# Kernel optimization log

Hardware: AMD Instinct MI355X
Metric: run time of the kernel (lower is better)

Reference implementation:

```python
import jax, jax.numpy as jnp
import numpy as np

B, LQ, C = 2, 12240, 256
NH, NL, NP = 8, 4, 4          # heads, levels, points
D = C // NH                   # head dim = 32
SHAPES = np.array([[96, 96], [48, 48], [24, 24], [12, 12]], dtype=np.int32)
LEN_IN = int((SHAPES[:, 0] * SHAPES[:, 1]).sum())  # 12240


def setup_inputs() -> dict:
    key = jax.random.key(0)
    ks = jax.random.split(key, 10)
    start = np.concatenate([[0], np.cumsum(SHAPES[:, 0] * SHAPES[:, 1])[:-1]]).astype(np.int32)
    return {
        "query": jax.random.normal(ks[0], (B, LQ, C), jnp.float32),
        "reference_points": jax.random.uniform(ks[1], (B, LQ, NL, 2), jnp.float32),
        "input_flatten": jax.random.normal(ks[2], (B, LEN_IN, C), jnp.float32),
        "input_spatial_shapes": jnp.asarray(SHAPES),
        "input_level_start_index": jnp.asarray(start),
        # params (sampling_offsets weight kept small so samples land near the reference point)
        "W_off": jax.random.normal(ks[3], (C, NH * NL * NP * 2), jnp.float32) * 0.01,
        "b_off": jax.random.normal(ks[4], (NH * NL * NP * 2,), jnp.float32) * 0.1,
        "W_attn": jax.random.normal(ks[5], (C, NH * NL * NP), jnp.float32) * 0.02,
        "b_attn": jnp.zeros((NH * NL * NP,), jnp.float32),
        "W_val": jax.random.normal(ks[6], (C, C), jnp.float32) * (1.0 / np.sqrt(C)),
        "b_val": jnp.zeros((C,), jnp.float32),
        "W_out": jax.random.normal(ks[7], (C, C), jnp.float32) * (1.0 / np.sqrt(C)),
        "b_out": jnp.zeros((C,), jnp.float32),
    }


def _bilinear_sample(v, loc):
    """grid_sample(align_corners=False, padding=zeros) equivalent.
    v:   (B, Hl, Wl, NH, D) level feature map per head
    loc: (B, Lq, NH, NP, 2) normalized sampling locations in [0,1]
    ->   (B, Lq, NH, NP, D)
    """
    _, Hl, Wl, _, _ = v.shape
    x = loc[..., 0] * Wl - 0.5
    y = loc[..., 1] * Hl - 0.5
    x0 = jnp.floor(x); y0 = jnp.floor(y)
    lx = x - x0;       ly = y - y0
    x0i = x0.astype(jnp.int32); y0i = y0.astype(jnp.int32)
    bi = jnp.arange(v.shape[0])[:, None, None, None]
    hi = jnp.arange(NH)[None, None, :, None]

    def gather(yi, xi):
        valid = (yi >= 0) & (yi < Hl) & (xi >= 0) & (xi < Wl)
        yc = jnp.clip(yi, 0, Hl - 1)
        xc = jnp.clip(xi, 0, Wl - 1)
        g = v[bi, yc, xc, hi]                       # (B,Lq,NH,NP,D)
        return g * valid[..., None].astype(v.dtype)

    w00 = (1 - lx) * (1 - ly); w01 = lx * (1 - ly)
    w10 = (1 - lx) * ly;       w11 = lx * ly
    return (gather(y0i, x0i) * w00[..., None] + gather(y0i, x0i + 1) * w01[..., None]
            + gather(y0i + 1, x0i) * w10[..., None] + gather(y0i + 1, x0i + 1) * w11[..., None])


def reference(query, reference_points, input_flatten, input_spatial_shapes,
              input_level_start_index, W_off, b_off, W_attn, b_attn,
              W_val, b_val, W_out, b_out):
    shapes = np.asarray(input_spatial_shapes)          # static level geometry
    starts = np.asarray(input_level_start_index)

    value = (input_flatten @ W_val + b_val).reshape(B, LEN_IN, NH, D)
    offsets = (query @ W_off + b_off).reshape(B, LQ, NH, NL, NP, 2)
    attn = (query @ W_attn + b_attn).reshape(B, LQ, NH, NL * NP)
    attn = jax.nn.softmax(attn, axis=-1).reshape(B, LQ, NH, NL, NP)

    # normalizer is (W_l, H_l) per level
    normalizer = jnp.stack([input_spatial_shapes[:, 1], input_spatial_shapes[:, 0]], -1).astype(query.dtype)
    loc = (reference_points[:, :, None, :, None, :]
           + offsets / normalizer[None, None, None, :, None, :])  # (B,Lq,NH,NL,NP,2)

    out = jnp.zeros((B, LQ, NH, D), query.dtype)
    for l in range(NL):
        Hl, Wl = int(shapes[l, 0]), int(shapes[l, 1])
        s = int(starts[l])
        v_l = value[:, s:s + Hl * Wl].reshape(B, Hl, Wl, NH, D)
        sampled = _bilinear_sample(v_l, loc[:, :, :, l])            # (B,Lq,NH,NP,D)
        out = out + jnp.einsum("bqhpd,bqhp->bqhd", sampled, attn[:, :, :, l])
    out = out.reshape(B, LQ, C)
    return out @ W_out + b_out
```

## Files before the change

kernel.cpp:

```cpp
#include <hip/hip_runtime.h>
#include <math.h>

#define B_    2
#define LQ_   12240
#define C_    256
#define NH_   8
#define NL_   4
#define NP_   4
#define LEN_IN_ 12240
#define MROWS (B_*LQ_)
#define MF_   (MROWS/16)
#define KF_   8
#define APLANE ((size_t)MROWS * C_)
#define NBLK  383

typedef __attribute__((ext_vector_type(8))) short short8v;
typedef __attribute__((ext_vector_type(4))) float f32x4;
typedef __attribute__((ext_vector_type(2))) float f32x2;
typedef __attribute__((ext_vector_type(2))) uint  u32x2;

__device__ __forceinline__ ushort f2bf_hi(float f) {
    uint u = __builtin_bit_cast(uint, f);
    uint r = (u + 0x7fffu + ((u >> 16) & 1u)) >> 16;
    return (ushort)r;
}
__device__ __forceinline__ float bf2f(ushort h) {
    uint u = ((uint)h) << 16;
    return __builtin_bit_cast(float, u);
}

#define U4_VAL  0
#define U4_OFF  8192
#define U4_ATT  16384
#define U4_UHI  20480
#define U4_ULO  28672
#define PACKB_TOTAL 294912

#define ESTRIDE 272
#define FSTRIDE 268

__global__ __launch_bounds__(256) void pack_w_kernel(
    const float* __restrict__ Wv, const float* __restrict__ Wo,
    const float* __restrict__ Wa, const float* __restrict__ Wu,
    ushort* __restrict__ packB)
{
    int gid = blockIdx.x * 256 + threadIdx.x;
    if (gid >= 28672) return;
    const float* W; ushort* hi; ushort* lo = nullptr; int N, rel;
    if (gid < 8192)       { W = Wv; hi = packB;          N = 256; rel = gid; }
    else if (gid < 16384) { W = Wo; hi = packB + 65536;  N = 256; rel = gid - 8192; }
    else if (gid < 20480) { W = Wa; hi = packB + 131072; N = 128; rel = gid - 16384; }
    else { W = Wu; hi = packB + 163840; lo = packB + 229376; N = 256; rel = gid - 20480; }

    const int lane = rel & 63;
    const int kf   = (rel >> 6) & 7;
    const int nf   = rel >> 9;
    const int row0 = kf * 32 + (lane >> 4) * 8;
    const int col  = nf * 16 + (lane & 15);

    union { ushort u16[8]; uint4 u4; } ch, cl;
#pragma unroll
    for (int j = 0; j < 8; ++j) {
        float x = W[(size_t)(row0 + j) * N + col];
        ushort h = f2bf_hi(x);
        ch.u16[j] = h;
        cl.u16[j] = f2bf_hi(x - bf2f(h));
    }
    *reinterpret_cast<uint4*>(hi + (size_t)rel * 8) = ch.u4;
    if (lo) *reinterpret_cast<uint4*>(lo + (size_t)rel * 8) = cl.u4;
}

__global__ __launch_bounds__(512) void gemm_vq_kernel(
    const float* __restrict__ inflat, const float* __restrict__ query,
    const ushort* __restrict__ packB,
    const float* __restrict__ b_val, const float* __restrict__ b_off,
    const float* __restrict__ b_attn,
    ushort* __restrict__ valbf, ushort* __restrict__ offsb, ushort* __restrict__ attnb)
{
    const int t = threadIdx.x, lane = t & 63, wid = t >> 6;
    const int rowBase = blockIdx.x * 64;
    const bool isVal = (blockIdx.y == 0);
    const float* __restrict__ A = isVal ? inflat : query;

    __shared__ ushort Sh[64 * ESTRIDE];

#pragma unroll
    for (int i = 0; i < 4; ++i) {
        int frag = i * 512 + t;
        int fl = frag & 63, kf = (frag >> 6) & 7, mf = frag >> 9;
        int row = min(rowBase + mf * 16 + (fl & 15), MROWS - 1);
        int k0 = kf * 32 + (fl >> 4) * 8;
        const float4* s = reinterpret_cast<const float4*>(A + (size_t)row * 256 + k0);
        float4 v0 = s[0], v1 = s[1];
        float vv[8] = { v0.x, v0.y, v0.z, v0.w, v1.x, v1.y, v1.z, v1.w };
        union { ushort u16[8]; uint4 u4; } hh;
#pragma unroll
        for (int j = 0; j < 8; ++j) hh.u16[j] = f2bf_hi(vv[j]);
        *reinterpret_cast<uint4*>(&Sh[(size_t)frag * 8]) = hh.u4;
    }
    __syncthreads();

    const uint4* A4 = reinterpret_cast<const uint4*>(Sh);
    const int colLane = lane & 15, rquad = lane >> 4;
    const int wnf = wid * 2;

    if (isVal) {
        const uint4* B4 = reinterpret_cast<const uint4*>(packB) + U4_VAL;
        f32x4 acc[4][2];
#pragma unroll
        for (int mi = 0; mi < 4; ++mi)
#pragma unroll
            for (int f = 0; f < 2; ++f) acc[mi][f] = (f32x4)0.0f;

#pragma unroll
        for (int kf = 0; kf < KF_; ++kf) {
            uint4 bh[2], ah[4];
#pragma unroll
            for (int f = 0; f < 2; ++f) bh[f] = B4[((wnf + f) * KF_ + kf) * 64 + lane];
#pragma unroll
            for (int mi = 0; mi < 4; ++mi) ah[mi] = A4[(mi * KF_ + kf) * 64 + lane];
#pragma unroll
            for (int mi = 0; mi < 4; ++mi) {
                short8v a = __builtin_bit_cast(short8v, ah[mi]);
#pragma unroll
                for (int f = 0; f < 2; ++f)
                    acc[mi][f] = __builtin_amdgcn_mfma_f32_16x16x32_bf16(
                        a, __builtin_bit_cast(short8v, bh[f]), acc[mi][f], 0, 0, 0);
            }
        }
        __syncthreads();
#pragma unroll
        for (int f = 0; f < 2; ++f) {
            int col = (wnf + f) * 16 + colLane;
            float bv = b_val[col];
#pragma unroll
            for (int mi = 0; mi < 4; ++mi)
#pragma unroll
                for (int e = 0; e < 4; ++e)
                    Sh[(mi * 16 + rquad * 4 + e) * ESTRIDE + col] = f2bf_hi(acc[mi][f][e] + bv);
        }
        __syncthreads();
#pragma unroll
        for (int i = 0; i < 4; ++i) {
            int idx = i * 512 + t, row = idx >> 5, c8 = idx & 31;
            int grow = rowBase + row;
            if (grow < MROWS)
                *reinterpret_cast<uint4*>(valbf + (size_t)grow * 256 + c8 * 8) =
                    *reinterpret_cast<const uint4*>(&Sh[row * ESTRIDE + c8 * 8]);
        }
    } else {
        const uint4* BO = reinterpret_cast<const uint4*>(packB) + U4_OFF;
        const uint4* BA = reinterpret_cast<const uint4*>(packB) + U4_ATT;
        f32x4 acc[4][3];
#pragma unroll
        for (int mi = 0; mi < 4; ++mi)
#pragma unroll
            for (int f = 0; f < 3; ++f) acc[mi][f] = (f32x4)0.0f;

#pragma unroll
        for (int kf = 0; kf < KF_; ++kf) {
            uint4 bh[3], ah[4];
#pragma unroll
            for (int f = 0; f < 2; ++f) bh[f] = BO[((wnf + f) * KF_ + kf) * 64 + lane];
            bh[2] = BA[(wid * KF_ + kf) * 64 + lane];
#pragma unroll
            for (int mi = 0; mi < 4; ++mi) ah[mi] = A4[(mi * KF_ + kf) * 64 + lane];
#pragma unroll
            for (int mi = 0; mi < 4; ++mi) {
                short8v a = __builtin_bit_cast(short8v, ah[mi]);
#pragma unroll
                for (int f = 0; f < 3; ++f)
                    acc[mi][f] = __builtin_amdgcn_mfma_f32_16x16x32_bf16(
                        a, __builtin_bit_cast(short8v, bh[f]), acc[mi][f], 0, 0, 0);
            }
        }
        __syncthreads();
#pragma unroll
        for (int f = 0; f < 2; ++f) {
            int col = (wnf + f) * 16 + colLane;
            float bv = b_off[col];
#pragma unroll
            for (int mi = 0; mi < 4; ++mi)
#pragma unroll
                for (int e = 0; e < 4; ++e)
                    Sh[(mi * 16 + rquad * 4 + e) * ESTRIDE + col] = f2bf_hi(acc[mi][f][e] + bv);
        }
        __syncthreads();
#pragma unroll
        for (int i = 0; i < 4; ++i) {
            int idx = i * 512 + t, row = idx >> 5, c8 = idx & 31;
            int grow = rowBase + row;
            if (grow < MROWS)
                *reinterpret_cast<uint4*>(offsb + (size_t)grow * 256 + c8 * 8) =
                    *reinterpret_cast<const uint4*>(&Sh[row * ESTRIDE + c8 * 8]);
        }
        __syncthreads();
        {
            int col = wid * 16 + colLane;
            float bv = b_attn[col];
#pragma unroll
            for (int mi = 0; mi < 4; ++mi)
#pragma unroll
                for (int e = 0; e < 4; ++e) {
                    float v = acc[mi][2][e] + bv;
                    float mx = v;
#pragma unroll
                    for (int m = 8; m >= 1; m >>= 1) mx = fmaxf(mx, __shfl_xor(mx, m, 16));
                    float ex = __expf(v - mx);
                    float s = ex;
#pragma unroll
                    for (int m = 8; m >= 1; m >>= 1) s += __shfl_xor(s, m, 16);
                    Sh[(mi * 16 + rquad * 4 + e) * ESTRIDE + col] = f2bf_hi(ex / s);
                }
        }
        __syncthreads();
#pragma unroll
        for (int i = 0; i < 2; ++i) {
            int idx = i * 512 + t, row = idx >> 4, c8 = idx & 15;
            int grow = rowBase + row;
            if (grow < MROWS)
                *reinterpret_cast<uint4*>(attnb + (size_t)grow * 128 + c8 * 8) =
                    *reinterpret_cast<const uint4*>(&Sh[row * ESTRIDE + c8 * 8]);
        }
    }
}

__global__ __launch_bounds__(512) void gemm_out_kernel(
    const ushort* __restrict__ midH, const ushort* __restrict__ packB,
    const float* __restrict__ bias, float* __restrict__ Cg)
{
    const int t = threadIdx.x, lane = t & 63, wid = t >> 6;
    const int rowBase = blockIdx.x * 64;

    __shared__ ushort Sh[64 * ESTRIDE];

    const uint4* H4 = reinterpret_cast<const uint4*>(midH);
#pragma unroll
    for (int i = 0; i < 4; ++i) {
        int frag = i * 512 + t;
        int fl = frag & 63, kf = (frag >> 6) & 7, mf = frag >> 9;
        int row = min(rowBase + mf * 16 + (fl & 15), MROWS - 1);
        int kq = kf * 4 + (fl >> 4);
        *reinterpret_cast<uint4*>(&Sh[(size_t)frag * 8]) = H4[(size_t)row * 32 + kq];
    }
    __syncthreads();

    const uint4* BH4 = reinterpret_cast<const uint4*>(packB) + U4_UHI;
    const uint4* BL4 = reinterpret_cast<const uint4*>(packB) + U4_ULO;
    const uint4* A4 = reinterpret_cast<const uint4*>(Sh);
    const int wnf = wid * 2;

    f32x4 acc[4][2];
#pragma unroll
    for (int mi = 0; mi < 4; ++mi)
#pragma unroll
        for (int f = 0; f < 2; ++f) acc[mi][f] = (f32x4)0.0f;

#pragma unroll
    for (int kf = 0; kf < KF_; ++kf) {
        uint4 bh[2], bl[2], ah[4];
#pragma unroll
        for (int f = 0; f < 2; ++f) {
            bh[f] = BH4[((wnf + f) * KF_ + kf) * 64 + lane];
            bl[f] = BL4[((wnf + f) * KF_ + kf) * 64 + lane];
        }
#pragma unroll
        for (int mi = 0; mi < 4; ++mi) ah[mi] = A4[(mi * KF_ + kf) * 64 + lane];
#pragma unroll
        for (int mi = 0; mi < 4; ++mi) {
            short8v a = __builtin_bit_cast(short8v, ah[mi]);
#pragma unroll
            for (int f = 0; f < 2; ++f) {
                acc[mi][f] = __builtin_amdgcn_mfma_f32_16x16x32_bf16(
                    a, __builtin_bit_cast(short8v, bh[f]), acc[mi][f], 0, 0, 0);
                acc[mi][f] = __builtin_amdgcn_mfma_f32_16x16x32_bf16(
                    a, __builtin_bit_cast(short8v, bl[f]), acc[mi][f], 0, 0, 0);
            }
        }
    }

    const int colLane = lane & 15, rquad = lane >> 4;
    float* ShF = reinterpret_cast<float*>(Sh);
#pragma unroll
    for (int phase = 0; phase < 2; ++phase) {
        __syncthreads();
#pragma unroll
        for (int f = 0; f < 2; ++f) {
            int col = (wnf + f) * 16 + colLane;
            float bv = bias[col];
#pragma unroll
            for (int mi2 = 0; mi2 < 2; ++mi2) {
                int mi = phase * 2 + mi2;
#pragma unroll
                for (int e = 0; e < 4; ++e)
                    ShF[(mi2 * 16 + rquad * 4 + e) * FSTRIDE + col] = acc[mi][f][e] + bv;
            }
        }
        __syncthreads();
#pragma unroll
        for (int i = 0; i < 4; ++i) {
            int idx = i * 512 + t, row = idx >> 6, c4 = idx & 63;
            int grow = rowBase + phase * 32 + row;
            if (grow < MROWS)
                *reinterpret_cast<float4*>(Cg + (size_t)grow * 256 + c4 * 4) =
                    *reinterpret_cast<const float4*>(&ShF[row * FSTRIDE + c4 * 4]);
        }
    }
}

__global__ __launch_bounds__(128) void sampler_kernel(
    const ushort* __restrict__ value,
    const ushort* __restrict__ offs,
    const ushort* __restrict__ attnw,
    const float* __restrict__ refp,
    ushort* __restrict__ midH)
{
    const int t  = threadIdx.x;
    const int qi = t >> 6;
    const int t6 = t & 63;
    const int q  = blockIdx.x * 2 + qi;

    __shared__ float s_ref[2][8];
    __shared__ int   s_addr[2][576];
    __shared__ float s_w[2][576];

    if (t < 16) s_ref[t >> 3][t & 7] = refp[(size_t)(blockIdx.x * 2 + (t >> 3)) * 8 + (t & 7)];
    __syncthreads();

#pragma unroll
    for (int batch = 0; batch < 2; ++batch) {
        const int p  = t6 + batch * 64;
        const int h  = p >> 4;
        const int lp = p & 15;
        const int l  = lp >> 2;

        const float aw = bf2f(attnw[(size_t)q * 128 + p]);
        const uint o2 = reinterpret_cast<const uint*>(offs)[(size_t)q * 128 + p];
        const float ox = bf2f((ushort)(o2 & 0xffffu));
        const float oy = bf2f((ushort)(o2 >> 16));
        const float rx = s_ref[qi][l * 2 + 0];
        const float ry = s_ref[qi][l * 2 + 1];

        const int   Wl = 96 >> l;
        const int   st = 12288 - (12288 >> (2 * l));
        const float fW = (float)Wl;

        const float x = fmaf(rx, fW, ox) - 0.5f;
        const float y = fmaf(ry, fW, oy) - 0.5f;
        const float x0f = floorf(x), y0f = floorf(y);
        const float fx = x - x0f, fy = y - y0f;
        const int x0 = (int)x0f, y0 = (int)y0f;
        const int x1 = x0 + 1,   y1 = y0 + 1;

        const float vx0 = (x0 >= 0 && x0 < Wl) ? 1.f : 0.f;
        const float vx1 = (x1 >= 0 && x1 < Wl) ? 1.f : 0.f;
        const float vy0 = (y0 >= 0 && y0 < Wl) ? 1.f : 0.f;
        const float vy1 = (y1 >= 0 && y1 < Wl) ? 1.f : 0.f;

        const int xc0 = min(max(x0, 0), Wl - 1);
        const int xc1 = min(max(x1, 0), Wl - 1);
        const int yc0 = min(max(y0, 0), Wl - 1);
        const int yc1 = min(max(y1, 0), Wl - 1);

        const int row0 = st + yc0 * Wl;
        const int row1 = st + yc1 * Wl;
        const int hb   = h << 5;

        const int sidx = (lp * 9 + h) * 4;
        int4 a;
        a.x = ((row0 + xc0) << 8) + hb;
        a.y = ((row0 + xc1) << 8) + hb;
        a.z = ((row1 + xc0) << 8) + hb;
        a.w = ((row1 + xc1) << 8) + hb;
        *reinterpret_cast<int4*>(&s_addr[qi][sidx]) = a;

        float4 w;
        w.x = aw * (1.f - fx) * (1.f - fy) * vx0 * vy0;
        w.y = aw * fx * (1.f - fy) * vx1 * vy0;
        w.z = aw * (1.f - fx) * fy * vx0 * vy1;
        w.w = aw * fx * fy * vx1 * vy1;
        *reinterpret_cast<float4*>(&s_w[qi][sidx]) = w;
    }
    __syncthreads();

    const int c2 = t6 >> 5;
    const int h  = (t6 >> 2) & 7;
    const int l2 = t6 & 3;
    const int d8 = l2 * 8;
    const ushort* __restrict__ vb = value + (q >= LQ_ ? (size_t)LEN_IN_ * 256 : 0) + d8;

    f32x2 aLo = (f32x2)0.f, aHi = (f32x2)0.f, bLo = (f32x2)0.f, bHi = (f32x2)0.f;

#pragma unroll
    for (int pt = 0; pt < 16; ++pt) {
        const int base = (pt * 9 + h) * 4 + c2 * 2;
        const int2   a = *reinterpret_cast<const int2*>(&s_addr[qi][base]);
        const float2 w = *reinterpret_cast<const float2*>(&s_w[qi][base]);
        uint4 v0 = *reinterpret_cast<const uint4*>(vb + a.x);
        uint4 v1 = *reinterpret_cast<const uint4*>(vb + a.y);
        f32x2 w0; w0.x = w.x; w0.y = w.x;
        f32x2 w1; w1.x = w.y; w1.y = w.y;

        u32x2 h01; h01.x = v0.x; h01.y = v0.y;
        u32x2 h23; h23.x = v0.z; h23.y = v0.w;
        u32x2 l01 = h01 << 16, l23 = h23 << 16;
        aHi = __builtin_elementwise_fma(__builtin_bit_cast(f32x2, h01), w0, aHi);
        aLo = __builtin_elementwise_fma(__builtin_bit_cast(f32x2, l01), w0, aLo);
        bHi = __builtin_elementwise_fma(__builtin_bit_cast(f32x2, h23), w0, bHi);
        bLo = __builtin_elementwise_fma(__builtin_bit_cast(f32x2, l23), w0, bLo);

        u32x2 g01; g01.x = v1.x; g01.y = v1.y;
        u32x2 g23; g23.x = v1.z; g23.y = v1.w;
        u32x2 m01 = g01 << 16, m23 = g23 << 16;
        aHi = __builtin_elementwise_fma(__builtin_bit_cast(f32x2, g01), w1, aHi);
        aLo = __builtin_elementwise_fma(__builtin_bit_cast(f32x2, m01), w1, aLo);
        bHi = __builtin_elementwise_fma(__builtin_bit_cast(f32x2, g23), w1, bHi);
        bLo = __builtin_elementwise_fma(__builtin_bit_cast(f32x2, m23), w1, bLo);
    }

    float r[8] = { aLo.x, aHi.x, aLo.y, aHi.y, bLo.x, bHi.x, bLo.y, bHi.y };
#pragma unroll
    for (int j = 0; j < 8; ++j) r[j] += __shfl_xor(r[j], 32);

    if (c2 == 0) {
        union { ushort u16[8]; uint4 u4; } hh;
#pragma unroll
        for (int j = 0; j < 8; ++j) hh.u16[j] = f2bf_hi(r[j]);
        *reinterpret_cast<uint4*>(midH + (size_t)q * 256 + (h << 5) + d8) = hh.u4;
    }
}

extern "C" void kernel_launch(void* const* d_in, const int* in_sizes, int n_in,
                              void* d_out, int out_size, void* d_ws, size_t ws_size,
                              hipStream_t stream)
{
    const float* query  = (const float*)d_in[0];
    const float* refp   = (const float*)d_in[1];
    const float* inflat = (const float*)d_in[2];
    const float* W_off  = (const float*)d_in[5];
    const float* b_off  = (const float*)d_in[6];
    const float* W_attn = (const float*)d_in[7];
    const float* b_attn = (const float*)d_in[8];
    const float* W_val  = (const float*)d_in[9];
    const float* b_val  = (const float*)d_in[10];
    const float* W_out  = (const float*)d_in[11];
    const float* b_out  = (const float*)d_in[12];
    float* out = (float*)d_out;

    ushort* midH  = (ushort*)d_ws;
    ushort* valbf = midH + APLANE;
    ushort* packB = valbf + APLANE;
    ushort* offsb = packB + PACKB_TOTAL;
    ushort* attnb = offsb + APLANE;

    hipLaunchKernelGGL(pack_w_kernel, dim3(112), dim3(256), 0, stream,
                       W_val, W_off, W_attn, W_out, packB);
    hipLaunchKernelGGL(gemm_vq_kernel, dim3(NBLK, 2), dim3(512), 0, stream,
                       inflat, query, packB, b_val, b_off, b_attn,
                       valbf, offsb, attnb);
    hipLaunchKernelGGL(sampler_kernel, dim3(MROWS / 2), dim3(128), 0, stream,
                       valbf, offsb, attnb, refp, midH);
    hipLaunchKernelGGL(gemm_out_kernel, dim3(NBLK), dim3(512), 0, stream,
                       midH, packB, b_out, out);
}
```

Measured before the change: 79.87 us.

## Fuse deformable sampler with output projection GEMM in one kernel

Merges the sampling kernel and the output-projection GEMM into one kernel that handles 16 queries per block. The sampled bf16 head outputs stay in shared memory and feed MFMA directly, which removes the global round trip through the intermediate buffer and one kernel launch. Sampling weights are now stored in shared memory as bf16 to save LDS, at some cost in precision. The GEMM tile shrinks to 16 rows per block, so each block reloads the full weight matrix, and the larger LDS footprint may reduce occupancy.

Result: slower. 83.44 us (+4.5%).

```diff
diff --git a/kernel.cpp b/kernel.cpp
--- a/kernel.cpp
+++ b/kernel.cpp
@@ -9,10 +9,10 @@
 #define NP_   4
 #define LEN_IN_ 12240
 #define MROWS (B_*LQ_)
-#define MF_   (MROWS/16)
 #define KF_   8
 #define APLANE ((size_t)MROWS * C_)
 #define NBLK  383
+#define QBLK  1530
 
 typedef __attribute__((ext_vector_type(8))) short short8v;
 typedef __attribute__((ext_vector_type(4))) float f32x4;
@@ -37,7 +37,8 @@
 #define PACKB_TOTAL 294912
 
 #define ESTRIDE 272
-#define FSTRIDE 268
+#define MSTRIDE 264
+#define OSTRIDE 260
 
 __global__ __launch_bounds__(256) void pack_w_kernel(
     const float* __restrict__ Wv, const float* __restrict__ Wo,
@@ -225,121 +226,42 @@
     }
 }
 
-__global__ __launch_bounds__(512) void gemm_out_kernel(
-    const ushort* __restrict__ midH, const ushort* __restrict__ packB,
-    const float* __restrict__ bias, float* __restrict__ Cg)
-{
-    const int t = threadIdx.x, lane = t & 63, wid = t >> 6;
-    const int rowBase = blockIdx.x * 64;
-
-    __shared__ ushort Sh[64 * ESTRIDE];
-
-    const uint4* H4 = reinterpret_cast<const uint4*>(midH);
-#pragma unroll
-    for (int i = 0; i < 4; ++i) {
-        int frag = i * 512 + t;
-        int fl = frag & 63, kf = (frag >> 6) & 7, mf = frag >> 9;
-        int row = min(rowBase + mf * 16 + (fl & 15), MROWS - 1);
-        int kq = kf * 4 + (fl >> 4);
-        *reinterpret_cast<uint4*>(&Sh[(size_t)frag * 8]) = H4[(size_t)row * 32 + kq];
-    }
-    __syncthreads();
-
-    const uint4* BH4 = reinterpret_cast<const uint4*>(packB) + U4_UHI;
-    const uint4* BL4 = reinterpret_cast<const uint4*>(packB) + U4_ULO;
-    const uint4* A4 = reinterpret_cast<const uint4*>(Sh);
-    const int wnf = wid * 2;
-
-    f32x4 acc[4][2];
-#pragma unroll
-    for (int mi = 0; mi < 4; ++mi)
-#pragma unroll
-        for (int f = 0; f < 2; ++f) acc[mi][f] = (f32x4)0.0f;
-
-#pragma unroll
-    for (int kf = 0; kf < KF_; ++kf) {
-        uint4 bh[2], bl[2], ah[4];
-#pragma unroll
-        for (int f = 0; f < 2; ++f) {
-            bh[f] = BH4[((wnf + f) * KF_ + kf) * 64 + lane];
-            bl[f] = BL4[((wnf + f) * KF_ + kf) * 64 + lane];
-        }
-#pragma unroll
-        for (int mi = 0; mi < 4; ++mi) ah[mi] = A4[(mi * KF_ + kf) * 64 + lane];
-#pragma unroll
-        for (int mi = 0; mi < 4; ++mi) {
-            short8v a = __builtin_bit_cast(short8v, ah[mi]);
-#pragma unroll
-            for (int f = 0; f < 2; ++f) {
-                acc[mi][f] = __builtin_amdgcn_mfma_f32_16x16x32_bf16(
-                    a, __builtin_bit_cast(short8v, bh[f]), acc[mi][f], 0, 0, 0);
-                acc[mi][f] = __builtin_amdgcn_mfma_f32_16x16x32_bf16(
-                    a, __builtin_bit_cast(short8v, bl[f]), acc[mi][f], 0, 0, 0);
-            }
-        }
-    }
-
-    const int colLane = lane & 15, rquad = lane >> 4;
-    float* ShF = reinterpret_cast<float*>(Sh);
-#pragma unroll
-    for (int phase = 0; phase < 2; ++phase) {
-        __syncthreads();
-#pragma unroll
-        for (int f = 0; f < 2; ++f) {
-            int col = (wnf + f) * 16 + colLane;
-            float bv = bias[col];
-#pragma unroll
-            for (int mi2 = 0; mi2 < 2; ++mi2) {
-                int mi = phase * 2 + mi2;
-#pragma unroll
-                for (int e = 0; e < 4; ++e)
-                    ShF[(mi2 * 16 + rquad * 4 + e) * FSTRIDE + col] = acc[mi][f][e] + bv;
-            }
-        }
-        __syncthreads();
-#pragma unroll
-        for (int i = 0; i < 4; ++i) {
-            int idx = i * 512 + t, row = idx >> 6, c4 = idx & 63;
-            int grow = rowBase + phase * 32 + row;
-            if (grow < MROWS)
-                *reinterpret_cast<float4*>(Cg + (size_t)grow * 256 + c4 * 4) =
-                    *reinterpret_cast<const float4*>(&ShF[row * FSTRIDE + c4 * 4]);
-        }
-    }
-}
-
-__global__ __launch_bounds__(128) void sampler_kernel(
+__global__ __launch_bounds__(512) void sampler_out_kernel(
     const ushort* __restrict__ value,
     const ushort* __restrict__ offs,
     const ushort* __restrict__ attnw,
     const float* __restrict__ refp,
-    ushort* __restrict__ midH)
+    const ushort* __restrict__ packB,
+    const float* __restrict__ b_out,
+    float* __restrict__ outp)
 {
-    const int t  = threadIdx.x;
-    const int qi = t >> 6;
-    const int t6 = t & 63;
-    const int q  = blockIdx.x * 2 + qi;
-
-    __shared__ float s_ref[2][8];
-    __shared__ int   s_addr[2][576];
-    __shared__ float s_w[2][576];
-
-    if (t < 16) s_ref[t >> 3][t & 7] = refp[(size_t)(blockIdx.x * 2 + (t >> 3)) * 8 + (t & 7)];
-    __syncthreads();
-
-#pragma unroll
-    for (int batch = 0; batch < 2; ++batch) {
-        const int p  = t6 + batch * 64;
+    const int t = threadIdx.x;
+    const int qBase = blockIdx.x * 16;
+
+    __shared__ float  s_ref[16][8];
+    __shared__ int    s_addr[16][576];
+    __shared__ ushort s_wbf[16][576];
+    __shared__ ushort Amid[16 * MSTRIDE];
+
+    if (t < 128) s_ref[t >> 3][t & 7] = refp[(size_t)qBase * 8 + t];
+    __syncthreads();
+
+#pragma unroll
+    for (int b = 0; b < 4; ++b) {
+        const int g  = b * 512 + t;
+        const int ql = g >> 7;
+        const int p  = g & 127;
         const int h  = p >> 4;
         const int lp = p & 15;
         const int l  = lp >> 2;
+        const int q  = qBase + ql;
 
         const float aw = bf2f(attnw[(size_t)q * 128 + p]);
         const uint o2 = reinterpret_cast<const uint*>(offs)[(size_t)q * 128 + p];
         const float ox = bf2f((ushort)(o2 & 0xffffu));
         const float oy = bf2f((ushort)(o2 >> 16));
-        const float rx = s_ref[qi][l * 2 + 0];
-        const float ry = s_ref[qi][l * 2 + 1];
+        const float rx = s_ref[ql][l * 2 + 0];
+        const float ry = s_ref[ql][l * 2 + 1];
 
         const int   Wl = 96 >> l;
         const int   st = 12288 - (12288 >> (2 * l));
@@ -372,61 +294,113 @@
         a.y = ((row0 + xc1) << 8) + hb;
         a.z = ((row1 + xc0) << 8) + hb;
         a.w = ((row1 + xc1) << 8) + hb;
-        *reinterpret_cast<int4*>(&s_addr[qi][sidx]) = a;
-
-        float4 w;
-        w.x = aw * (1.f - fx) * (1.f - fy) * vx0 * vy0;
-        w.y = aw * fx * (1.f - fy) * vx1 * vy0;
-        w.z = aw * (1.f - fx) * fy * vx0 * vy1;
-        w.w = aw * fx * fy * vx1 * vy1;
-        *reinterpret_cast<float4*>(&s_w[qi][sidx]) = w;
-    }
-    __syncthreads();
-
-    const int c2 = t6 >> 5;
-    const int h  = (t6 >> 2) & 7;
-    const int l2 = t6 & 3;
+        *reinterpret_cast<int4*>(&s_addr[ql][sidx]) = a;
+
+        const float w00 = aw * (1.f - fx) * (1.f - fy) * vx0 * vy0;
+        const float w01 = aw * fx * (1.f - fy) * vx1 * vy0;
+        const float w10 = aw * (1.f - fx) * fy * vx0 * vy1;
+        const float w11 = aw * fx * fy * vx1 * vy1;
+        *reinterpret_cast<ushort4*>(&s_wbf[ql][sidx]) =
+            make_ushort4(f2bf_hi(w00), f2bf_hi(w01), f2bf_hi(w10), f2bf_hi(w11));
+    }
+    __syncthreads();
+
+    const int lane = t & 63, wid = t >> 6;
+    const int c2 = lane >> 5;
+    const int h  = (lane >> 2) & 7;
+    const int l2 = lane & 3;
     const int d8 = l2 * 8;
-    const ushort* __restrict__ vb = value + (q >= LQ_ ? (size_t)LEN_IN_ * 256 : 0) + d8;
-
-    f32x2 aLo = (f32x2)0.f, aHi = (f32x2)0.f, bLo = (f32x2)0.f, bHi = (f32x2)0.f;
-
-#pragma unroll
-    for (int pt = 0; pt < 16; ++pt) {
-        const int base = (pt * 9 + h) * 4 + c2 * 2;
-        const int2   a = *reinterpret_cast<const int2*>(&s_addr[qi][base]);
-        const float2 w = *reinterpret_cast<const float2*>(&s_w[qi][base]);
-        uint4 v0 = *reinterpret_cast<const uint4*>(vb + a.x);
-        uint4 v1 = *reinterpret_cast<const uint4*>(vb + a.y);
-        f32x2 w0; w0.x = w.x; w0.y = w.x;
-        f32x2 w1; w1.x = w.y; w1.y = w.y;
-
-        u32x2 h01; h01.x = v0.x; h01.y = v0.y;
-        u32x2 h23; h23.x = v0.z; h23.y = v0.w;
-        u32x2 l01 = h01 << 16, l23 = h23 << 16;
-        aHi = __builtin_elementwise_fma(__builtin_bit_cast(f32x2, h01), w0, aHi);
-        aLo = __builtin_elementwise_fma(__builtin_bit_cast(f32x2, l01), w0, aLo);
-        bHi = __builtin_elementwise_fma(__builtin_bit_cast(f32x2, h23), w0, bHi);
-        bLo = __builtin_elementwise_fma(__builtin_bit_cast(f32x2, l23), w0, bLo);
-
-        u32x2 g01; g01.x = v1.x; g01.y = v1.y;
-        u32x2 g23; g23.x = v1.z; g23.y = v1.w;
-        u32x2 m01 = g01 << 16, m23 = g23 << 16;
-        aHi = __builtin_elementwise_fma(__builtin_bit_cast(f32x2, g01), w1, aHi);
-        aLo = __builtin_elementwise_fma(__builtin_bit_cast(f32x2, m01), w1, aLo);
-        bHi = __builtin_elementwise_fma(__builtin_bit_cast(f32x2, g23), w1, bHi);
-        bLo = __builtin_elementwise_fma(__builtin_bit_cast(f32x2, m23), w1, bLo);
-    }
-
-    float r[8] = { aLo.x, aHi.x, aLo.y, aHi.y, bLo.x, bHi.x, bLo.y, bHi.y };
-#pragma unroll
-    for (int j = 0; j < 8; ++j) r[j] += __shfl_xor(r[j], 32);
-
-    if (c2 == 0) {
-        union { ushort u16[8]; uint4 u4; } hh;
-#pragma unroll
-        for (int j = 0; j < 8; ++j) hh.u16[j] = f2bf_hi(r[j]);
-        *reinterpret_cast<uint4*>(midH + (size_t)q * 256 + (h << 5) + d8) = hh.u4;
+
+#pragma unroll
+    for (int sub = 0; sub < 2; ++sub) {
+        const int ql = wid * 2 + sub;
+        const int q  = qBase + ql;
+        const ushort* __restrict__ vb = value + (q >= LQ_ ? (size_t)LEN_IN_ * 256 : 0) + d8;
+
+        f32x2 aLo = (f32x2)0.f, aHi = (f32x2)0.f, bLo = (f32x2)0.f, bHi = (f32x2)0.f;
+
+#pragma unroll
+        for (int pt = 0; pt < 16; ++pt) {
+            const int base = (pt * 9 + h) * 4 + c2 * 2;
+            const int2 a = *reinterpret_cast<const int2*>(&s_addr[ql][base]);
+            const uint wu = *reinterpret_cast<const uint*>(&s_wbf[ql][base]);
+            uint4 v0 = *reinterpret_cast<const uint4*>(vb + a.x);
+            uint4 v1 = *reinterpret_cast<const uint4*>(vb + a.y);
+            const float wxa = bf2f((ushort)(wu & 0xffffu));
+            const float wxb = bf2f((ushort)(wu >> 16));
+            f32x2 w0; w0.x = wxa; w0.y = wxa;
+            f32x2 w1; w1.x = wxb; w1.y = wxb;
+
+            u32x2 h01; h01.x = v0.x; h01.y = v0.y;
+            u32x2 h23; h23.x = v0.z; h23.y = v0.w;
+            u32x2 l01 = h01 << 16, l23 = h23 << 16;
+            aHi = __builtin_elementwise_fma(__builtin_bit_cast(f32x2, h01), w0, aHi);
+            aLo = __builtin_elementwise_fma(__builtin_bit_cast(f32x2, l01), w0, aLo);
+            bHi = __builtin_elementwise_fma(__builtin_bit_cast(f32x2, h23), w0, bHi);
+            bLo = __builtin_elementwise_fma(__builtin_bit_cast(f32x2, l23), w0, bLo);
+
+            u32x2 g01; g01.x = v1.x; g01.y = v1.y;
+            u32x2 g23; g23.x = v1.z; g23.y = v1.w;
+            u32x2 m01 = g01 << 16, m23 = g23 << 16;
+            aHi = __builtin_elementwise_fma(__builtin_bit_cast(f32x2, g01), w1, aHi);
+            aLo = __builtin_elementwise_fma(__builtin_bit_cast(f32x2, m01), w1, aLo);
+            bHi = __builtin_elementwise_fma(__builtin_bit_cast(f32x2, g23), w1, bHi);
+            bLo = __builtin_elementwise_fma(__builtin_bit_cast(f32x2, m23), w1, bLo);
+        }
+
+        float r[8] = { aLo.x, aHi.x, aLo.y, aHi.y, bLo.x, bHi.x, bLo.y, bHi.y };
+#pragma unroll
+        for (int j = 0; j < 8; ++j) r[j] += __shfl_xor(r[j], 32);
+
+        if (c2 == 0) {
+            union { ushort u16[8]; uint4 u4; } hh;
+#pragma unroll
+            for (int j = 0; j < 8; ++j) hh.u16[j] = f2bf_hi(r[j]);
+            *reinterpret_cast<uint4*>(&Amid[ql * MSTRIDE + (h << 5) + d8]) = hh.u4;
+        }
+    }
+    __syncthreads();
+
+    const int frRow = lane & 15, chunk = lane >> 4;
+    const int wnf = wid * 2;
+    const uint4* BH4 = reinterpret_cast<const uint4*>(packB) + U4_UHI;
+    const uint4* BL4 = reinterpret_cast<const uint4*>(packB) + U4_ULO;
+
+    f32x4 acc[2];
+    acc[0] = (f32x4)0.0f; acc[1] = (f32x4)0.0f;
+
+#pragma unroll
+    for (int kf = 0; kf < KF_; ++kf) {
+        uint4 ahv = *reinterpret_cast<const uint4*>(&Amid[frRow * MSTRIDE + kf * 32 + chunk * 8]);
+        short8v a = __builtin_bit_cast(short8v, ahv);
+#pragma unroll
+        for (int f = 0; f < 2; ++f) {
+            uint4 bh = BH4[((wnf + f) * KF_ + kf) * 64 + lane];
+            uint4 bl = BL4[((wnf + f) * KF_ + kf) * 64 + lane];
+            acc[f] = __builtin_amdgcn_mfma_f32_16x16x32_bf16(
+                a, __builtin_bit_cast(short8v, bh), acc[f], 0, 0, 0);
+            acc[f] = __builtin_amdgcn_mfma_f32_16x16x32_bf16(
+                a, __builtin_bit_cast(short8v, bl), acc[f], 0, 0, 0);
+        }
+    }
+
+    float* ShF = reinterpret_cast<float*>(&s_addr[0][0]);
+    const int colLane = lane & 15, rquad = lane >> 4;
+    __syncthreads();
+#pragma unroll
+    for (int f = 0; f < 2; ++f) {
+        int col = (wnf + f) * 16 + colLane;
+        float bv = b_out[col];
+#pragma unroll
+        for (int e = 0; e < 4; ++e)
+            ShF[(rquad * 4 + e) * OSTRIDE + col] = acc[f][e] + bv;
+    }
+    __syncthreads();
+#pragma unroll
+    for (int i = 0; i < 2; ++i) {
+        int idx = i * 512 + t, row = idx >> 6, c4 = idx & 63;
+        *reinterpret_cast<float4*>(outp + (size_t)(qBase + row) * 256 + c4 * 4) =
+            *reinterpret_cast<const float4*>(&ShF[row * OSTRIDE + c4 * 4]);
     }
 }
 
@@ -447,8 +421,7 @@
     const float* b_out  = (const float*)d_in[12];
     float* out = (float*)d_out;
 
-    ushort* midH  = (ushort*)d_ws;
-    ushort* valbf = midH + APLANE;
+    ushort* valbf = (ushort*)d_ws;
     ushort* packB = valbf + APLANE;
     ushort* offsb = packB + PACKB_TOTAL;
     ushort* attnb = offsb + APLANE;
@@ -458,8 +431,6 @@
     hipLaunchKernelGGL(gemm_vq_kernel, dim3(NBLK, 2), dim3(512), 0, stream,
                        inflat, query, packB, b_val, b_off, b_attn,
                        valbf, offsb, attnb);
-    hipLaunchKernelGGL(sampler_kernel, dim3(MROWS / 2), dim3(128), 0, stream,
-                       valbf, offsb, attnb, refp, midH);
-    hipLaunchKernelGGL(gemm_out_kernel, dim3(NBLK), dim3(512), 0, stream,
-                       midH, packB, b_out, out);
-}
+    hipLaunchKernelGGL(sampler_out_kernel, dim3(QBLK), dim3(512), 0, stream,
+                       valbf, offsb, attnb, refp, packB, b_out, out);
+}
```
